# Kernel optimization log

Measured on AMD Instinct MI355X. Metric: run time of the kernel, lower is better.

Reference implementation:

```python
import jax, jax.numpy as jnp
import numpy as np

IN_CH = 31
OUT_CH = 31
G = 5          # grid_size
K = 3          # spline_order
GRID_LO, GRID_HI = -1.0, 1.0
NB = G + K     # number of B-spline basis functions
COEF_LEN = IN_CH * OUT_CH * NB        # 7688
UNIV_LEN = IN_CH * OUT_CH             # 961
RES_LEN = IN_CH * OUT_CH              # 961
PARAMS = COEF_LEN + UNIV_LEN + RES_LEN  # 9610


def _b_splines(x):
    """Cox-de Boor B-spline bases. x: (N, IN_CH) -> (N, IN_CH, G+K)."""
    h = (GRID_HI - GRID_LO) / G
    grid = jnp.arange(-K, G + K + 1, dtype=x.dtype) * h + GRID_LO  # (G+2K+1,)
    xe = x[..., None]
    b = ((xe >= grid[:-1]) & (xe < grid[1:])).astype(x.dtype)  # order-0, (N,I,G+2K)
    for p in range(1, K + 1):
        b = ((xe - grid[:-(p + 1)]) / (grid[p:-1] - grid[:-(p + 1)])) * b[..., :-1] \
          + ((grid[p + 1:] - xe) / (grid[p + 1:] - grid[1:-p])) * b[..., 1:]
    return b  # (N, IN_CH, NB)


def setup_inputs() -> dict:
    key = jax.random.key(0)
    k1, k2, k3 = jax.random.split(key, 3)
    # x in [-1,1) to span grid_range
    x = jax.random.uniform(k1, (1, IN_CH, 128, 128), dtype=jnp.float32) * 2.0 - 1.0
    # hypernetwork (generator) params: 3x3 conv 31 -> 9610
    gen_w = jax.random.normal(k2, (PARAMS, IN_CH, 3, 3), dtype=jnp.float32) * 0.02
    gen_b = jax.random.normal(k3, (PARAMS,), dtype=jnp.float32) * 0.01
    return {"x": x, "gen_w": gen_w, "gen_b": gen_b}


def reference(x, gen_w, gen_b):
    B, C, H, W = x.shape
    # generator: per-pixel KAN parameters, (B, PARAMS, H, W)
    w = jax.lax.conv_general_dilated(
        x, gen_w, window_strides=(1, 1), padding='SAME',
        dimension_numbers=('NCHW', 'OIHW', 'NCHW')) + gen_b[None, :, None, None]
    w = jnp.transpose(w, (0, 2, 3, 1)).reshape(B * H * W, PARAMS)
    xf = jnp.transpose(x, (0, 2, 3, 1)).reshape(B * H * W, C)
    # slice per-pixel params (mirrors kan_params_indices slicing + view)
    coef = w[:, :COEF_LEN].reshape(-1, IN_CH, OUT_CH, NB)
    univ = w[:, COEF_LEN:COEF_LEN + UNIV_LEN].reshape(-1, IN_CH, OUT_CH)
    res = w[:, COEF_LEN + UNIV_LEN:].reshape(-1, IN_CH, OUT_CH)
    bases = _b_splines(xf)                                # (N, I, NB)
    spline = jnp.einsum('nid,niod->nio', bases, coef)     # per-edge spline value
    silu = xf * jax.nn.sigmoid(xf)                        # residual activation
    out = jnp.einsum('nio,nio->no', univ, spline) + jnp.einsum('ni,nio->no', silu, res)
    return jnp.transpose(out.reshape(B, H, W, OUT_CH), (0, 3, 1, 2))
```

## Files before the change

kernel.cpp:

```cpp
#include <hip/hip_runtime.h>
#include <hip/hip_bf16.h>

#define OUT_CH   31
#define COEF_LEN 7688
#define NPIX     16384
#define CHUNKS   31
#define NFRG     24
#define NR       9
#define FRAG_U16 512
#define STEP_U16 (NFRG*FRAG_U16)
#define BP3_B    ((size_t)CHUNKS*NR*STEP_U16*2)
#define P1_B     ((size_t)OUT_CH*NPIX*4)
#define WS_NEED  (BP3_B + P1_B)

using f32x4 = __attribute__((ext_vector_type(4))) float;
using s16x8 = __attribute__((ext_vector_type(8))) short;

__device__ __forceinline__ unsigned short f2bf(float f) {
    unsigned int u = __float_as_uint(f);
    unsigned int r = (u + 0x7FFFu + ((u >> 16) & 1u)) >> 16;
    return (unsigned short)r;
}

__global__ void pack_kernel(const float* __restrict__ gw, const float* __restrict__ gb,
                            unsigned short* __restrict__ bp) {
    const int NMAIN = CHUNKS * NFRG * 64;
    int tt = blockIdx.x * 256 + threadIdx.x;
    if (tt >= NMAIN) return;
    int lane = tt & 63;
    int u = tt >> 6;
    int f = u % NFRG;
    int i = u / NFRG;
    int m = lane & 15, q8 = lane >> 4;
    int o = (m >> 2) * 8 + f / 3;
    int jslot = (f % 3) * 4 + (m & 3);
    int p = -1;
    if (o < OUT_CH && jslot < 10) {
        if (jslot < 8)       p = i * 248 + o * 8 + jslot;
        else if (jslot == 8) p = COEF_LEN + i * 31 + o;
        else                 p = COEF_LEN + 961 + i * 31 + o;
    }
    s16x8 vr[NR];
    #pragma unroll
    for (int r = 0; r < NR; ++r)
        #pragma unroll
        for (int jj = 0; jj < 8; ++jj) vr[r][jj] = 0;
    #pragma unroll
    for (int jj = 0; jj < 8; ++jj) {
        int ci = q8 * 8 + jj;
        if (p >= 0) {
            if (ci < 31) {
                const float* gr = gw + (long)p * 279 + ci * 9;
                #pragma unroll
                for (int r = 0; r < NR; ++r) vr[r][jj] = (short)f2bf(gr[r]);
            } else {
                vr[4][jj] = (short)f2bf(gb[p]);
            }
        }
    }
    #pragma unroll
    for (int r = 0; r < NR; ++r)
        *reinterpret_cast<s16x8*>(bp + (((size_t)i * NR + r) * NFRG + f) * FRAG_U16 + lane * 8) = vr[r];
}

__global__ void __launch_bounds__(512, 1)
main_kernel(const float* __restrict__ x, const unsigned short* __restrict__ bp3,
            float* __restrict__ dst0, float* __restrict__ dst1,
            int two_cg, int c0_in, int nc_in, int add_in) {
    __shared__ unsigned short slab[3 * 66 * 40];
    __shared__ float Wt[64 * 132];
    __shared__ unsigned short SLt[64 * 20];
    const int tid = threadIdx.x;
    const int bid = blockIdx.x;
    int row, ch, c0, nc, addf;
    float* dst;
    if (two_cg) {
        int cg = bid & 1;
        ch = (bid >> 1) & 1;
        row = bid >> 2;
        c0 = cg ? 16 : 0;
        nc = cg ? 15 : 16;
        dst = cg ? dst1 : dst0;
        addf = 0;
    } else {
        ch = bid & 1; row = bid >> 1;
        c0 = c0_in; nc = nc_in; dst = dst0; addf = add_in;
    }

    for (int idx = tid; idx < 3 * 66 * 40; idx += 512) {
        int slot = idx % 40;
        int t = idx / 40;
        int cc = t % 66;
        int rr = t / 66;
        int hh = row - 1 + rr, ww = ch * 64 - 1 + cc;
        unsigned short v = 0;
        if (slot < 31) {
            if ((unsigned)hh < 128u && (unsigned)ww < 128u)
                v = f2bf(x[slot * NPIX + hh * 128 + ww]);
        } else if (slot == 31) {
            v = 0x3F80;
        }
        slab[(rr * 66 + cc) * 40 + slot] = v;
    }

    for (int idx = tid; idx < nc * 64; idx += 512) {
        int px = idx & 63;
        int k = idx >> 6;
        float xv = x[(size_t)(c0 + k) * NPIX + row * 128 + ch * 64 + px];
        float u5 = (xv + 1.0f) * 2.5f;
        float cf = fminf(fmaxf(floorf(u5), 0.f), 4.f);
        int ccb = (int)cf;
        float t = u5 - cf;
        float omt = 1.f - t;
        float t2v = t * t, t3v = t2v * t;
        float bw0 = omt * omt * omt * (1.f / 6.f);
        float bw3 = t3v * (1.f / 6.f);
        float bw1 = 0.5f * t3v - t2v + (2.f / 3.f);
        float bw2 = 1.f - bw0 - bw1 - bw3;
        float* wr = Wt + px * 132 + k * 8;
        *reinterpret_cast<f32x4*>(wr) = (f32x4){0.f, 0.f, 0.f, 0.f};
        *reinterpret_cast<f32x4*>(wr + 4) = (f32x4){0.f, 0.f, 0.f, 0.f};
        wr[ccb] = bw0; wr[ccb + 1] = bw1; wr[ccb + 2] = bw2; wr[ccb + 3] = bw3;
        SLt[px * 20 + k] = f2bf(xv / (1.f + __expf(-xv)));
    }
    __syncthreads();

    const int lane = tid & 63;
    const int fi = tid >> 6;
    const int q = lane >> 4;
    const int pix16 = lane & 15;
    const char* slabb = (const char*)slab;

    int sa[4];
    #pragma unroll
    for (int pg = 0; pg < 4; ++pg)
        sa[pg] = (pg * 16 + pix16) * 80 + q * 16;

    float oreg[4] = {0.f, 0.f, 0.f, 0.f};

    #pragma unroll 1
    for (int k = 0; k < nc; ++k) {
        const unsigned short* aw = bp3
            + ((size_t)(c0 + k) * NR * NFRG + fi * 3) * FRAG_U16 + lane * 8;

        s16x8 pa[2][3];
        #pragma unroll
        for (int fl = 0; fl < 3; ++fl)
            pa[0][fl] = *reinterpret_cast<const s16x8*>(aw + fl * FRAG_U16);

        f32x4 acc[3][4];
        #pragma unroll
        for (int fl = 0; fl < 3; ++fl)
            #pragma unroll
            for (int pg = 0; pg < 4; ++pg)
                acc[fl][pg] = (f32x4){0.f, 0.f, 0.f, 0.f};

        #pragma unroll
        for (int r = 0; r < NR; ++r) {
            if (r + 1 < NR) {
                #pragma unroll
                for (int fl = 0; fl < 3; ++fl)
                    pa[(r + 1) & 1][fl] = *reinterpret_cast<const s16x8*>(
                        aw + (r + 1) * STEP_U16 + fl * FRAG_U16);
            }
            const int roff = ((r / 3) * 66 + (r % 3)) * 80;
            s16x8 pbv[4];
            #pragma unroll
            for (int pg = 0; pg < 4; ++pg)
                pbv[pg] = *reinterpret_cast<const s16x8*>(slabb + sa[pg] + roff);

            __builtin_amdgcn_s_setprio(1);
            #pragma unroll
            for (int fl = 0; fl < 3; ++fl)
                #pragma unroll
                for (int pg = 0; pg < 4; ++pg)
                    acc[fl][pg] = __builtin_amdgcn_mfma_f32_16x16x32_bf16(
                        pa[r & 1][fl], pbv[pg], acc[fl][pg], 0, 0, 0);
            __builtin_amdgcn_s_setprio(0);
        }

        #pragma unroll
        for (int pg = 0; pg < 4; ++pg) {
            const float* wr = Wt + (pg * 16 + pix16) * 132 + k * 8;
            f32x4 wlo = *reinterpret_cast<const f32x4*>(wr);
            f32x4 whi = *reinterpret_cast<const f32x4*>(wr + 4);
            unsigned short slb = SLt[(pg * 16 + pix16) * 20 + k];
            float sl = __uint_as_float((unsigned)slb << 16);
            float sp = wlo[0] * acc[0][pg][0];
            sp = fmaf(wlo[1], acc[0][pg][1], sp);
            sp = fmaf(wlo[2], acc[0][pg][2], sp);
            sp = fmaf(wlo[3], acc[0][pg][3], sp);
            sp = fmaf(whi[0], acc[1][pg][0], sp);
            sp = fmaf(whi[1], acc[1][pg][1], sp);
            sp = fmaf(whi[2], acc[1][pg][2], sp);
            sp = fmaf(whi[3], acc[1][pg][3], sp);
            oreg[pg] = fmaf(acc[2][pg][0], sp, fmaf(sl, acc[2][pg][1], oreg[pg]));
        }
    }

    const int o = q * 8 + fi;
    if (o < OUT_CH) {
        #pragma unroll
        for (int pg = 0; pg < 4; ++pg) {
            size_t gi = (size_t)o * NPIX + row * 128 + ch * 64 + pg * 16 + pix16;
            if (addf) dst[gi] += oreg[pg];
            else      dst[gi]  = oreg[pg];
        }
    }
}

__global__ void reduce_kernel(const float* __restrict__ p1, float* __restrict__ out) {
    int e = blockIdx.x * 256 + threadIdx.x;
    if (e < OUT_CH * NPIX) out[e] += p1[e];
}

extern "C" void kernel_launch(void* const* d_in, const int* in_sizes, int n_in,
                              void* d_out, int out_size, void* d_ws, size_t ws_size,
                              hipStream_t stream) {
    const float* x  = (const float*)d_in[0];
    const float* gw = (const float*)d_in[1];
    const float* gb = (const float*)d_in[2];
    float* outp = (float*)d_out;
    unsigned short* bpack = (unsigned short*)d_ws;
    float* p1 = (float*)((char*)d_ws + BP3_B);

    const int NMAIN = CHUNKS * NFRG * 64;
    pack_kernel<<<(NMAIN + 255) / 256, 256, 0, stream>>>(gw, gb, bpack);

    if (ws_size >= WS_NEED) {
        main_kernel<<<512, 512, 0, stream>>>(x, bpack, outp, p1, 1, 0, 0, 0);
        reduce_kernel<<<(OUT_CH * NPIX + 255) / 256, 256, 0, stream>>>(p1, outp);
    } else {
        main_kernel<<<256, 512, 0, stream>>>(x, bpack, outp, nullptr, 0, 0, 16, 0);
        main_kernel<<<256, 512, 0, stream>>>(x, bpack, outp, nullptr, 0, 16, 15, 1);
    }
}
```

Measured before the change: 109.3 us.

## Process a full image row per 1024-thread block to share weight fetches

Each block now handles a full 128-pixel row with 16 waves, where two half-row groups share the same packed generator weights, instead of separate blocks per half row. This halves global weight-fragment traffic per pixel and trims halo loading. It needs dynamic LDS above the static limit and halves the grid, which reduces scheduling flexibility and leaves one large block per CU.

```diff
diff --git a/kernel.cpp b/kernel.cpp
--- a/kernel.cpp
+++ b/kernel.cpp
@@ -12,6 +12,11 @@
 #define BP3_B    ((size_t)CHUNKS*NR*STEP_U16*2)
 #define P1_B     ((size_t)OUT_CH*NPIX*4)
 #define WS_NEED  (BP3_B + P1_B)
+
+#define SLAB_OFF  0
+#define WT_OFF    31200
+#define SLT_OFF   98784
+#define LDS_BYTES 103904
 
 using f32x4 = __attribute__((ext_vector_type(4))) float;
 using s16x8 = __attribute__((ext_vector_type(8))) short;
@@ -63,36 +68,37 @@
         *reinterpret_cast<s16x8*>(bp + (((size_t)i * NR + r) * NFRG + f) * FRAG_U16 + lane * 8) = vr[r];
 }
 
-__global__ void __launch_bounds__(512, 1)
+__global__ void __launch_bounds__(1024, 1)
 main_kernel(const float* __restrict__ x, const unsigned short* __restrict__ bp3,
             float* __restrict__ dst0, float* __restrict__ dst1,
             int two_cg, int c0_in, int nc_in, int add_in) {
-    __shared__ unsigned short slab[3 * 66 * 40];
-    __shared__ float Wt[64 * 132];
-    __shared__ unsigned short SLt[64 * 20];
+    extern __shared__ char smem[];
+    unsigned short* slab = (unsigned short*)(smem + SLAB_OFF);
+    float* Wt = (float*)(smem + WT_OFF);
+    unsigned short* SLt = (unsigned short*)(smem + SLT_OFF);
+
     const int tid = threadIdx.x;
     const int bid = blockIdx.x;
-    int row, ch, c0, nc, addf;
+    int row, c0, nc, addf;
     float* dst;
     if (two_cg) {
         int cg = bid & 1;
-        ch = (bid >> 1) & 1;
-        row = bid >> 2;
+        row = bid >> 1;
         c0 = cg ? 16 : 0;
         nc = cg ? 15 : 16;
         dst = cg ? dst1 : dst0;
         addf = 0;
     } else {
-        ch = bid & 1; row = bid >> 1;
+        row = bid;
         c0 = c0_in; nc = nc_in; dst = dst0; addf = add_in;
     }
 
-    for (int idx = tid; idx < 3 * 66 * 40; idx += 512) {
+    for (int idx = tid; idx < 3 * 130 * 40; idx += 1024) {
         int slot = idx % 40;
         int t = idx / 40;
-        int cc = t % 66;
-        int rr = t / 66;
-        int hh = row - 1 + rr, ww = ch * 64 - 1 + cc;
+        int cc = t % 130;
+        int rr = t / 130;
+        int hh = row - 1 + rr, ww = cc - 1;
         unsigned short v = 0;
         if (slot < 31) {
             if ((unsigned)hh < 128u && (unsigned)ww < 128u)
@@ -100,13 +106,13 @@
         } else if (slot == 31) {
             v = 0x3F80;
         }
-        slab[(rr * 66 + cc) * 40 + slot] = v;
-    }
-
-    for (int idx = tid; idx < nc * 64; idx += 512) {
-        int px = idx & 63;
-        int k = idx >> 6;
-        float xv = x[(size_t)(c0 + k) * NPIX + row * 128 + ch * 64 + px];
+        slab[(rr * 130 + cc) * 40 + slot] = v;
+    }
+
+    for (int idx = tid; idx < nc * 128; idx += 1024) {
+        int px = idx & 127;
+        int k = idx >> 7;
+        float xv = x[(size_t)(c0 + k) * NPIX + row * 128 + px];
         float u5 = (xv + 1.0f) * 2.5f;
         float cf = fminf(fmaxf(floorf(u5), 0.f), 4.f);
         int ccb = (int)cf;
@@ -126,7 +132,9 @@
     __syncthreads();
 
     const int lane = tid & 63;
-    const int fi = tid >> 6;
+    const int w = tid >> 6;
+    const int fi = w & 7;
+    const int ph = w >> 3;
     const int q = lane >> 4;
     const int pix16 = lane & 15;
     const char* slabb = (const char*)slab;
@@ -134,7 +142,7 @@
     int sa[4];
     #pragma unroll
     for (int pg = 0; pg < 4; ++pg)
-        sa[pg] = (pg * 16 + pix16) * 80 + q * 16;
+        sa[pg] = (ph * 64 + pg * 16 + pix16) * 80 + q * 16;
 
     float oreg[4] = {0.f, 0.f, 0.f, 0.f};
 
@@ -163,7 +171,7 @@
                     pa[(r + 1) & 1][fl] = *reinterpret_cast<const s16x8*>(
                         aw + (r + 1) * STEP_U16 + fl * FRAG_U16);
             }
-            const int roff = ((r / 3) * 66 + (r % 3)) * 80;
+            const int roff = ((r / 3) * 130 + (r % 3)) * 80;
             s16x8 pbv[4];
             #pragma unroll
             for (int pg = 0; pg < 4; ++pg)
@@ -181,10 +189,11 @@
 
         #pragma unroll
         for (int pg = 0; pg < 4; ++pg) {
-            const float* wr = Wt + (pg * 16 + pix16) * 132 + k * 8;
+            const int px = ph * 64 + pg * 16 + pix16;
+            const float* wr = Wt + px * 132 + k * 8;
             f32x4 wlo = *reinterpret_cast<const f32x4*>(wr);
             f32x4 whi = *reinterpret_cast<const f32x4*>(wr + 4);
-            unsigned short slb = SLt[(pg * 16 + pix16) * 20 + k];
+            unsigned short slb = SLt[px * 20 + k];
             float sl = __uint_as_float((unsigned)slb << 16);
             float sp = wlo[0] * acc[0][pg][0];
             sp = fmaf(wlo[1], acc[0][pg][1], sp);
@@ -202,7 +211,7 @@
     if (o < OUT_CH) {
         #pragma unroll
         for (int pg = 0; pg < 4; ++pg) {
-            size_t gi = (size_t)o * NPIX + row * 128 + ch * 64 + pg * 16 + pix16;
+            size_t gi = (size_t)o * NPIX + row * 128 + ph * 64 + pg * 16 + pix16;
             if (addf) dst[gi] += oreg[pg];
             else      dst[gi]  = oreg[pg];
         }
@@ -224,14 +233,17 @@
     unsigned short* bpack = (unsigned short*)d_ws;
     float* p1 = (float*)((char*)d_ws + BP3_B);
 
+    hipFuncSetAttribute((const void*)main_kernel,
+                        hipFuncAttributeMaxDynamicSharedMemorySize, LDS_BYTES);
+
     const int NMAIN = CHUNKS * NFRG * 64;
     pack_kernel<<<(NMAIN + 255) / 256, 256, 0, stream>>>(gw, gb, bpack);
 
     if (ws_size >= WS_NEED) {
-        main_kernel<<<512, 512, 0, stream>>>(x, bpack, outp, p1, 1, 0, 0, 0);
+        main_kernel<<<256, 1024, LDS_BYTES, stream>>>(x, bpack, outp, p1, 1, 0, 0, 0);
         reduce_kernel<<<(OUT_CH * NPIX + 255) / 256, 256, 0, stream>>>(p1, outp);
     } else {
-        main_kernel<<<256, 512, 0, stream>>>(x, bpack, outp, nullptr, 0, 0, 16, 0);
-        main_kernel<<<256, 512, 0, stream>>>(x, bpack, outp, nullptr, 0, 16, 15, 1);
-    }
-}
+        main_kernel<<<128, 1024, LDS_BYTES, stream>>>(x, bpack, outp, nullptr, 0, 0, 16, 0);
+        main_kernel<<<128, 1024, LDS_BYTES, stream>>>(x, bpack, outp, nullptr, 0, 16, 15, 1);
+    }
+}
```

Measured after the change: 107.9 us. About the same (-1.2%).
